# Performance work log

Measured on AMD Instinct MI355X. Metric: run time of the kernel, lower is better.

The kernel has to match this reference:

```python
import jax, jax.numpy as jnp
import numpy as np

B, M, I, J = 2, 8, 128, 64
DIM, HEADS, DIM_HEAD = 512, 8, 64
INNER = HEADS * DIM_HEAD
SCALE = DIM_HEAD ** -0.5


def setup_inputs() -> dict:
    key = jax.random.key(0)
    ks = jax.random.split(key, 8)
    x = jax.random.normal(ks[0], (B, M, I, DIM), dtype=jnp.float32)
    mems = jax.random.normal(ks[1], (B, M, I, J, DIM), dtype=jnp.float32)
    mask = jax.random.randint(ks[2], (B, M, I, J), 0, 2) > 0
    Wq = jax.random.normal(ks[3], (DIM, INNER), dtype=jnp.float32) * 0.02
    Wkv = jax.random.normal(ks[4], (DIM, 2 * INNER), dtype=jnp.float32) * 0.02
    Wo = jax.random.normal(ks[5], (INNER, DIM), dtype=jnp.float32) * 0.02
    bo = jnp.zeros((DIM,), dtype=jnp.float32)
    return {"x": x, "mems": mems, "mask": mask, "Wq": Wq, "Wkv": Wkv, "Wo": Wo, "bo": bo}


def _split_heads(t, h):
    # [..., h*d] -> [b, h, ..., d]  (head-major split of last dim)
    *lead, hd = t.shape
    d = hd // h
    t = t.reshape(*lead, h, d)
    # move head axis next to batch
    return jnp.moveaxis(t, -2, 1)


def reference(x, mems, mask, Wq, Wkv, Wo, bo):
    h = HEADS
    q = x @ Wq                       # [b, m, i, inner]
    kv = mems @ Wkv                  # [b, m, i, j, 2*inner]
    k, v = jnp.split(kv, 2, axis=-1)
    q = _split_heads(q, h) * SCALE   # [b, h, m, i, d]
    k = _split_heads(k, h)           # [b, h, m, i, j, d]
    v = _split_heads(v, h)
    # per-query memory attention scores
    sim = jnp.einsum('bhmid,bhmijd->bhmij', q, k)
    mask_value = -jnp.finfo(sim.dtype).max
    sim = jnp.where(mask[:, None], sim, mask_value)  # broadcast over heads
    attn = jax.nn.softmax(sim, axis=-1)
    out = jnp.einsum('bhmij,bhmijd->bhmid', attn, v)
    out = jnp.moveaxis(out, 1, -2)                   # [b, m, i, h, d]
    out = out.reshape(*out.shape[:-2], INNER)        # [b, m, i, inner]
    return out @ Wo + bo
```

## Files before the change

kernel.cpp:

```cpp
#include <hip/hip_runtime.h>
#include <cfloat>


#define SCALE 0.125f

__global__ __launch_bounds__(512) void k_clrb(
    const float* __restrict__ A, int lda, int a_hs,
    const float* __restrict__ B, int ldb, int bcol0,
    const float* __restrict__ bias, float alpha,
    float* __restrict__ C, int ldc, int K)
{
  const int t  = threadIdx.x;
  const int r0 = blockIdx.x * 8;
  int hoff = 0;
  if (a_hs) hoff = __builtin_amdgcn_readfirstlane(t >> 6) * a_hs;
  const float* a0 = A + (size_t)r0 * lda + hoff;
  const float* bp = B + bcol0 + t;
  float acc[8];
#pragma unroll
  for (int i = 0; i < 8; ++i) acc[i] = 0.f;
  for (int e = 0; e < K; e += 8) {
#pragma unroll
    for (int ee = 0; ee < 8; ++ee) {
      float bv = bp[(size_t)(e + ee) * ldb];
#pragma unroll
      for (int i = 0; i < 8; ++i)
        acc[i] += a0[(size_t)i * lda + e + ee] * bv;
    }
  }
  float bb = bias ? bias[t] : 0.f;
#pragma unroll
  for (int i = 0; i < 8; ++i)
    C[(size_t)(r0 + i) * ldc + t] = acc[i] * alpha + bb;
}

__global__ __launch_bounds__(512) void k_tmat(
    const float* __restrict__ Q, const float* __restrict__ Wkv,
    float* __restrict__ T)
{
  const int e  = threadIdx.x;
  const int r0 = blockIdx.x * 8;
  const int h  = blockIdx.y;
  const float* q0 = Q + (size_t)r0 * 512 + h * 64;
  const float* bp = Wkv + (size_t)e * 1024 + h * 64;
  float acc[8];
#pragma unroll
  for (int i = 0; i < 8; ++i) acc[i] = 0.f;
#pragma unroll
  for (int d = 0; d < 64; ++d) {
    float bv = bp[d];
#pragma unroll
    for (int i = 0; i < 8; ++i) acc[i] += q0[(size_t)i * 512 + d] * bv;
  }
  float* o = T + (size_t)r0 * 4096 + h * 512 + e;
#pragma unroll
  for (int i = 0; i < 8; ++i) o[(size_t)i * 4096] = acc[i];
}

__global__ __launch_bounds__(512, 4) void k_attn(
    const float* __restrict__ mems, const float* __restrict__ Tm,
    const int* __restrict__ mask, float* __restrict__ cbar)
{
  __shared__ float sm[13056];
  float* m_q  = sm;
  float* part = sm + 8448;
  float* p_s  = sm + 12544;

  const int t     = threadIdx.x;
  const int r     = blockIdx.x;
  const int j     = t & 63;
  const int cseg  = t >> 6;
  const int csegu = __builtin_amdgcn_readfirstlane(cseg);

  const float4* mrow =
      (const float4*)(mems + ((size_t)r * 64 + j) * 512 + cseg * 64);
  float4 mr[16];
#pragma unroll
  for (int i = 0; i < 16; ++i) mr[i] = mrow[i];

  const float* Trow = Tm + (size_t)r * 4096 + csegu * 64;
  float acc[8];
#pragma unroll
  for (int h = 0; h < 8; ++h) acc[h] = 0.f;
#pragma unroll
  for (int i = 0; i < 16; ++i) {
    float4 mv = mr[i];
#pragma unroll
    for (int h = 0; h < 8; ++h) {
      float4 tv = *(const float4*)(Trow + h * 512 + i * 4);
      acc[h] += mv.x * tv.x + mv.y * tv.y + mv.z * tv.z + mv.w * tv.w;
    }
  }
#pragma unroll
  for (int h = 0; h < 8; ++h) part[cseg * 512 + h * 64 + j] = acc[h];
  __syncthreads();

  {
    const int h = cseg;
    float s = 0.f;
#pragma unroll
    for (int cs = 0; cs < 8; ++cs) s += part[cs * 512 + h * 64 + j];
    const bool mk = mask[(size_t)r * 64 + j] != 0;
    s = mk ? s : -FLT_MAX;
    float mx = s;
#pragma unroll
    for (int o = 32; o > 0; o >>= 1) mx = fmaxf(mx, __shfl_xor(mx, o));
    float ev = mk ? __expf(s - mx) : 0.f;
    float l = ev;
#pragma unroll
    for (int o = 32; o > 0; o >>= 1) l += __shfl_xor(l, o);
    p_s[j * 8 + h] = ev / l;
  }
  __syncthreads();

  const int cc = t & 127;
  const int jh = t >> 7;
  for (int q = 0; q < 4; ++q) {
    if ((cseg >> 1) == q) {
      float* dst = m_q + j * 132 + (cseg & 1) * 64;
#pragma unroll
      for (int i = 0; i < 16; ++i) *(float4*)(dst + i * 4) = mr[i];
    }
    __syncthreads();
    float cb[8];
#pragma unroll
    for (int h = 0; h < 8; ++h) cb[h] = 0.f;
#pragma unroll
    for (int k = 0; k < 16; ++k) {
      const int jj = jh * 16 + k;
      float  mv = m_q[jj * 132 + cc];
      float4 pa = *(const float4*)(p_s + jj * 8);
      float4 pb = *(const float4*)(p_s + jj * 8 + 4);
      cb[0] += pa.x * mv; cb[1] += pa.y * mv; cb[2] += pa.z * mv; cb[3] += pa.w * mv;
      cb[4] += pb.x * mv; cb[5] += pb.y * mv; cb[6] += pb.z * mv; cb[7] += pb.w * mv;
    }
#pragma unroll
    for (int h = 0; h < 8; ++h) part[(jh * 8 + h) * 128 + cc] = cb[h];
    __syncthreads();
#pragma unroll
    for (int w = 0; w < 2; ++w) {
      const int idx = t + w * 512;
      const int h  = idx >> 7;
      const int c2 = idx & 127;
      float v = part[(0 * 8 + h) * 128 + c2] + part[(1 * 8 + h) * 128 + c2] +
                part[(2 * 8 + h) * 128 + c2] + part[(3 * 8 + h) * 128 + c2];
      cbar[(size_t)r * 4096 + h * 512 + q * 128 + c2] = v;
    }
    __syncthreads();
  }
}

extern "C" void kernel_launch(void* const* d_in, const int* in_sizes, int n_in,
                              void* d_out, int out_size, void* d_ws, size_t ws_size,
                              hipStream_t stream)
{
  const float* x    = (const float*)d_in[0];
  const float* mems = (const float*)d_in[1];
  const int*   mask = (const int*)  d_in[2];
  const float* Wq   = (const float*)d_in[3];
  const float* Wkv  = (const float*)d_in[4];
  const float* Wo   = (const float*)d_in[5];
  const float* bo   = (const float*)d_in[6];
  float* out = (float*)d_out;

  float* Q  = (float*)d_ws;
  float* Tm = Q  + (size_t)2048 * 512;
  float* cb = Tm + (size_t)2048 * 4096;
  float* O  = cb + (size_t)2048 * 4096;

  k_clrb<<<256, 512, 0, stream>>>(x, 512, 0, Wq, 512, 0, nullptr, SCALE, Q, 512, 512);
  k_tmat<<<dim3(256, 8), 512, 0, stream>>>(Q, Wkv, Tm);
  k_attn<<<2048, 512, 0, stream>>>(mems, Tm, mask, cb);
  k_clrb<<<256, 512, 0, stream>>>(cb, 4096, 512, Wkv, 1024, 512, nullptr, 1.f, O, 512, 512);
  k_clrb<<<256, 512, 0, stream>>>(O, 512, 0, Wo, 512, 0, bo, 1.f, out, 512, 512);
}
```

Measured before the change: 615.3 us.

## Transpose K weights for coalesced T-matrix loads and widen attention blocks to 1024 threads

Adds a kernel that transposes the K half of Wkv so the T-matrix kernel reads weights with consecutive threads hitting consecutive addresses, instead of a 4 KB stride per thread. The attention kernel now uses 1024 threads per row. Each thread holds 32 channels of mems in registers instead of 64, and the weighted-sum pass runs in two 256-column chunks instead of four 128-column chunks. This is meant to cut register pressure, expose more memory parallelism on the large mems stream, and halve the barrier rounds. The cost is a larger shared-memory footprint, an extra reduction stage, and half the threads idle during the softmax step.

```diff
diff --git a/kernel.cpp b/kernel.cpp
--- a/kernel.cpp
+++ b/kernel.cpp
@@ -34,21 +34,42 @@
     C[(size_t)(r0 + i) * ldc + t] = acc[i] * alpha + bb;
 }
 
+__global__ __launch_bounds__(256) void k_transpose(
+    const float* __restrict__ Wkv, float* __restrict__ Wkt)
+{
+  __shared__ float tile[64][65];
+  const int lx = threadIdx.x & 63;
+  const int ly = threadIdx.x >> 6;
+  const int bx = blockIdx.x;
+  const int by = blockIdx.y;
+#pragma unroll
+  for (int i = 0; i < 16; ++i) {
+    const int y = ly + i * 4;
+    tile[y][lx] = Wkv[(size_t)(by * 64 + y) * 1024 + bx * 64 + lx];
+  }
+  __syncthreads();
+#pragma unroll
+  for (int i = 0; i < 16; ++i) {
+    const int y = ly + i * 4;
+    Wkt[(size_t)(bx * 64 + y) * 512 + by * 64 + lx] = tile[lx][y];
+  }
+}
+
 __global__ __launch_bounds__(512) void k_tmat(
-    const float* __restrict__ Q, const float* __restrict__ Wkv,
+    const float* __restrict__ Q, const float* __restrict__ Wkt,
     float* __restrict__ T)
 {
   const int e  = threadIdx.x;
   const int r0 = blockIdx.x * 8;
   const int h  = blockIdx.y;
   const float* q0 = Q + (size_t)r0 * 512 + h * 64;
-  const float* bp = Wkv + (size_t)e * 1024 + h * 64;
+  const float* bp = Wkt + (size_t)h * 64 * 512 + e;
   float acc[8];
 #pragma unroll
   for (int i = 0; i < 8; ++i) acc[i] = 0.f;
 #pragma unroll
   for (int d = 0; d < 64; ++d) {
-    float bv = bp[d];
+    float bv = bp[(size_t)d * 512];
 #pragma unroll
     for (int i = 0; i < 8; ++i) acc[i] += q0[(size_t)i * 512 + d] * bv;
   }
@@ -57,33 +78,33 @@
   for (int i = 0; i < 8; ++i) o[(size_t)i * 4096] = acc[i];
 }
 
-__global__ __launch_bounds__(512, 4) void k_attn(
+__global__ __launch_bounds__(1024, 4) void k_attn(
     const float* __restrict__ mems, const float* __restrict__ Tm,
     const int* __restrict__ mask, float* __restrict__ cbar)
 {
-  __shared__ float sm[13056];
+  __shared__ float sm[16640 + 8192 + 512];
   float* m_q  = sm;
-  float* part = sm + 8448;
-  float* p_s  = sm + 12544;
+  float* part = sm + 16640;
+  float* p_s  = sm + 16640 + 8192;
 
-  const int t     = threadIdx.x;
-  const int r     = blockIdx.x;
-  const int j     = t & 63;
-  const int cseg  = t >> 6;
-  const int csegu = __builtin_amdgcn_readfirstlane(cseg);
+  const int t   = threadIdx.x;
+  const int r   = blockIdx.x;
+  const int j   = t & 63;
+  const int cs  = t >> 6;
+  const int csu = __builtin_amdgcn_readfirstlane(cs);
 
   const float4* mrow =
-      (const float4*)(mems + ((size_t)r * 64 + j) * 512 + cseg * 64);
-  float4 mr[16];
+      (const float4*)(mems + ((size_t)r * 64 + j) * 512 + cs * 32);
+  float4 mr[8];
 #pragma unroll
-  for (int i = 0; i < 16; ++i) mr[i] = mrow[i];
+  for (int i = 0; i < 8; ++i) mr[i] = mrow[i];
 
-  const float* Trow = Tm + (size_t)r * 4096 + csegu * 64;
+  const float* Trow = Tm + (size_t)r * 4096 + csu * 32;
   float acc[8];
 #pragma unroll
   for (int h = 0; h < 8; ++h) acc[h] = 0.f;
 #pragma unroll
-  for (int i = 0; i < 16; ++i) {
+  for (int i = 0; i < 8; ++i) {
     float4 mv = mr[i];
 #pragma unroll
     for (int h = 0; h < 8; ++h) {
@@ -92,14 +113,14 @@
     }
   }
 #pragma unroll
-  for (int h = 0; h < 8; ++h) part[cseg * 512 + h * 64 + j] = acc[h];
+  for (int h = 0; h < 8; ++h) part[cs * 512 + h * 64 + j] = acc[h];
   __syncthreads();
 
-  {
-    const int h = cseg;
+  if (t < 512) {
+    const int h = cs & 7;
     float s = 0.f;
 #pragma unroll
-    for (int cs = 0; cs < 8; ++cs) s += part[cs * 512 + h * 64 + j];
+    for (int c2 = 0; c2 < 16; ++c2) s += part[c2 * 512 + h * 64 + j];
     const bool mk = mask[(size_t)r * 64 + j] != 0;
     s = mk ? s : -FLT_MAX;
     float mx = s;
@@ -113,13 +134,13 @@
   }
   __syncthreads();
 
-  const int cc = t & 127;
-  const int jh = t >> 7;
-  for (int q = 0; q < 4; ++q) {
-    if ((cseg >> 1) == q) {
-      float* dst = m_q + j * 132 + (cseg & 1) * 64;
+  const int cc = t & 255;
+  const int jh = t >> 8;
+  for (int q = 0; q < 2; ++q) {
+    if ((cs >> 3) == q) {
+      float* dst = m_q + j * 260 + (cs & 7) * 32;
 #pragma unroll
-      for (int i = 0; i < 16; ++i) *(float4*)(dst + i * 4) = mr[i];
+      for (int i = 0; i < 8; ++i) *(float4*)(dst + i * 4) = mr[i];
     }
     __syncthreads();
     float cb[8];
@@ -128,23 +149,23 @@
 #pragma unroll
     for (int k = 0; k < 16; ++k) {
       const int jj = jh * 16 + k;
-      float  mv = m_q[jj * 132 + cc];
+      float  mv = m_q[jj * 260 + cc];
       float4 pa = *(const float4*)(p_s + jj * 8);
       float4 pb = *(const float4*)(p_s + jj * 8 + 4);
       cb[0] += pa.x * mv; cb[1] += pa.y * mv; cb[2] += pa.z * mv; cb[3] += pa.w * mv;
       cb[4] += pb.x * mv; cb[5] += pb.y * mv; cb[6] += pb.z * mv; cb[7] += pb.w * mv;
     }
 #pragma unroll
-    for (int h = 0; h < 8; ++h) part[(jh * 8 + h) * 128 + cc] = cb[h];
+    for (int h = 0; h < 8; ++h) part[(jh * 8 + h) * 256 + cc] = cb[h];
     __syncthreads();
 #pragma unroll
     for (int w = 0; w < 2; ++w) {
-      const int idx = t + w * 512;
-      const int h  = idx >> 7;
-      const int c2 = idx & 127;
-      float v = part[(0 * 8 + h) * 128 + c2] + part[(1 * 8 + h) * 128 + c2] +
-                part[(2 * 8 + h) * 128 + c2] + part[(3 * 8 + h) * 128 + c2];
-      cbar[(size_t)r * 4096 + h * 512 + q * 128 + c2] = v;
+      const int idx = t + w * 1024;
+      const int h   = idx >> 8;
+      const int c2  = idx & 255;
+      float v = part[(0 * 8 + h) * 256 + c2] + part[(1 * 8 + h) * 256 + c2] +
+                part[(2 * 8 + h) * 256 + c2] + part[(3 * 8 + h) * 256 + c2];
+      cbar[(size_t)r * 4096 + h * 512 + q * 256 + c2] = v;
     }
     __syncthreads();
   }
@@ -163,14 +184,16 @@
   const float* bo   = (const float*)d_in[6];
   float* out = (float*)d_out;
 
-  float* Q  = (float*)d_ws;
-  float* Tm = Q  + (size_t)2048 * 512;
-  float* cb = Tm + (size_t)2048 * 4096;
-  float* O  = cb + (size_t)2048 * 4096;
+  float* Q   = (float*)d_ws;
+  float* Tm  = Q   + (size_t)2048 * 512;
+  float* cb  = Tm  + (size_t)2048 * 4096;
+  float* O   = cb  + (size_t)2048 * 4096;
+  float* Wkt = O   + (size_t)2048 * 512;
 
+  k_transpose<<<dim3(8, 8), 256, 0, stream>>>(Wkv, Wkt);
   k_clrb<<<256, 512, 0, stream>>>(x, 512, 0, Wq, 512, 0, nullptr, SCALE, Q, 512, 512);
-  k_tmat<<<dim3(256, 8), 512, 0, stream>>>(Q, Wkv, Tm);
-  k_attn<<<2048, 512, 0, stream>>>(mems, Tm, mask, cb);
+  k_tmat<<<dim3(256, 8), 512, 0, stream>>>(Q, Wkt, Tm);
+  k_attn<<<2048, 1024, 0, stream>>>(mems, Tm, mask, cb);
   k_clrb<<<256, 512, 0, stream>>>(cb, 4096, 512, Wkv, 1024, 512, nullptr, 1.f, O, 512, 512);
   k_clrb<<<256, 512, 0, stream>>>(O, 512, 0, Wo, 512, 0, bo, 1.f, out, 512, 512);
 }
```

New measurement: 636.5 us. 1.03x slower.
